# Performance work log

Hardware: AMD Instinct MI355X
Metric: run time of the kernel (lower is better)

Reference implementation:

```python
import jax, jax.numpy as jnp
import numpy as np

N_WORD, N_TOPIC, N_DOC = 50000, 2000, 50000
D_WORD, D_TOPIC, D_OUT = 256, 128, 128
E_WW, E_WT, E_WD, E_TD, E_TT = 500000, 400000, 500000, 400000, 300000


def setup_inputs() -> dict:
    key = jax.random.key(0)
    ks = jax.random.split(key, 32)
    i = iter(range(32))

    def randn(shape, scale=1.0):
        return jax.random.normal(ks[next(i)], shape, dtype=jnp.float32) * scale

    def edges(n_e, n_src, n_dst):
        src = jax.random.randint(ks[next(i)], (n_e,), 0, n_src, dtype=jnp.int32)
        dst = jax.random.randint(ks[next(i)], (n_e,), 0, n_dst, dtype=jnp.int32)
        w = jax.random.uniform(ks[next(i)], (n_e,), dtype=jnp.float32)
        return src, dst, w

    feat_word = randn((N_WORD, D_WORD))
    feat_topic = randn((N_TOPIC, D_TOPIC))
    ww_src, ww_dst, ww_w = edges(E_WW, N_WORD, N_WORD)
    wt_src, wt_dst, wt_w = edges(E_WT, N_WORD, N_TOPIC)
    wd_src, wd_dst, wd_w = edges(E_WD, N_WORD, N_DOC)
    td_src, td_dst, td_w = edges(E_TD, N_TOPIC, N_DOC)
    tt_src, tt_dst, tt_w = edges(E_TT, N_TOPIC, N_TOPIC)
    return dict(
        feat_word=feat_word, feat_topic=feat_topic,
        ww_src=ww_src, ww_dst=ww_dst, ww_w=ww_w,
        wt_src=wt_src, wt_dst=wt_dst, wt_w=wt_w,
        wd_src=wd_src, wd_dst=wd_dst, wd_w=wd_w,
        td_src=td_src, td_dst=td_dst, td_w=td_w,
        tt_src=tt_src, tt_dst=tt_dst, tt_w=tt_w,
        W_ww=randn((D_WORD, D_OUT), 0.02), b_ww=randn((D_OUT,), 0.02),
        W_wt=randn((D_WORD, D_OUT), 0.02), b_wt=randn((D_OUT,), 0.02),
        W_wd=randn((D_WORD, D_OUT), 0.02), b_wd=randn((D_OUT,), 0.02),
        W_td=randn((D_TOPIC, D_OUT), 0.02), b_td=randn((D_OUT,), 0.02),
        W_tt=randn((D_TOPIC, D_OUT), 0.02), b_tt=randn((D_OUT,), 0.02),
    )


def _mean_agg(Wh, src, dst, w, n_dst):
    # u_mul_e: gather src feature, scale by edge weight; fn.mean: divide by in-degree
    m = Wh[src] * w[:, None]                                   # [E, D_OUT]
    s = jax.ops.segment_sum(m, dst, num_segments=n_dst)        # [n_dst, D_OUT]
    deg = jax.ops.segment_sum(jnp.ones_like(w), dst, num_segments=n_dst)
    return jnp.where(deg[:, None] > 0, s / jnp.maximum(deg, 1.0)[:, None], 0.0)


def reference(feat_word, feat_topic,
              ww_src, ww_dst, ww_w, wt_src, wt_dst, wt_w,
              wd_src, wd_dst, wd_w, td_src, td_dst, td_w,
              tt_src, tt_dst, tt_w,
              W_ww, b_ww, W_wt, b_wt, W_wd, b_wd, W_td, b_td, W_tt, b_tt):
    # Per-relation projections (note: in the torch source the causal/noise
    # branches are overwritten by the plain Linear, so this is the effective math).
    Wh_ww = feat_word @ W_ww + b_ww
    Wh_wt = feat_word @ W_wt + b_wt
    Wh_wd = feat_word @ W_wd + b_wd
    Wh_td = feat_topic @ W_td + b_td
    Wh_tt = feat_topic @ W_tt + b_tt
    # mean per edge type, then cross-etype 'sum' per destination node type
    h_word = _mean_agg(Wh_ww, ww_src, ww_dst, ww_w, N_WORD)
    h_topic = (_mean_agg(Wh_wt, wt_src, wt_dst, wt_w, N_TOPIC)
               + _mean_agg(Wh_tt, tt_src, tt_dst, tt_w, N_TOPIC))
    h_doc = (_mean_agg(Wh_wd, wd_src, wd_dst, wd_w, N_DOC)
             + _mean_agg(Wh_td, td_src, td_dst, td_w, N_DOC))
    return h_word, h_topic, h_doc
```

## Files before the change

### kernel.cpp

```cpp
#include <hip/hip_runtime.h>

typedef short short8 __attribute__((ext_vector_type(8)));
typedef float floatx4 __attribute__((ext_vector_type(4)));

__device__ __forceinline__ float b2f(unsigned int u16) {
    union { unsigned int i; float f; } v;
    v.i = u16 << 16;
    return v.f;
}
__device__ __forceinline__ unsigned short f2b(float f) {
    unsigned int i = __float_as_uint(f);
    unsigned int r = (i + 0x7FFFu + ((i >> 16) & 1u)) >> 16;
    return (unsigned short)r;
}

#define N_WORD  50000
#define N_TOPIC 2000
#define N_DOC   50000
#define CHAIN_END 0xFFFFFFFFu
#define NB_GEMM 814
#define NSLOT_WW (N_WORD * 8)
#define NSLOT_WT (N_TOPIC * 4)
#define NSLOT_TT (N_TOPIC * 4)
#define NSLOT_WD (N_DOC * 8)
#define NSLOT_TD (N_DOC * 8)
#define NSLOT_ALL (NSLOT_WW + NSLOT_WT + NSLOT_TT + NSLOT_WD + NSLOT_TD)

__global__ void detect_kernel(const unsigned int* __restrict__ feat_u32,
                              unsigned int* __restrict__ flag)
{
    int cnt = 0;
    for (int i = 0; i < 256; ++i) {
        unsigned int u = feat_u32[i];
        int e = (u >> 7) & 0xFF;
        if (e >= 110 && e <= 140) ++cnt;
    }
    *flag = (cnt > 128) ? 1u : 0u;
}

__global__ __launch_bounds__(256) void swizzle_kernel(
    const void* __restrict__ W0, const void* __restrict__ W1,
    const void* __restrict__ W2, const void* __restrict__ W3,
    const void* __restrict__ W4,
    const void* __restrict__ b0, const void* __restrict__ b1,
    const void* __restrict__ b2, const void* __restrict__ b3,
    const void* __restrict__ b4,
    short8* __restrict__ D0, short8* __restrict__ D1,
    short8* __restrict__ D2, short8* __restrict__ D3,
    short8* __restrict__ D4,
    unsigned short* __restrict__ bias_out,
    const unsigned int* __restrict__ flag_p)
{
    const int w = blockIdx.y;
    const void* W; const void* bs; short8* D; int S;
    switch (w) {
        case 0: W = W0; bs = b0; D = D0; S = 8; break;
        case 1: W = W1; bs = b1; D = D1; S = 8; break;
        case 2: W = W2; bs = b2; D = D2; S = 8; break;
        case 3: W = W3; bs = b3; D = D3; S = 4; break;
        default: W = W4; bs = b4; D = D4; S = 4; break;
    }
    const int n_entries = S * 8 * 64;
    const int mode = (int)*flag_p;
    for (int e = blockIdx.x * 256 + threadIdx.x; e < n_entries; e += 8 * 256) {
        const int lane = e & 63, t = (e >> 6) & 7, s = e >> 9;
        const int q = lane >> 4, n = t * 16 + (lane & 15);
        short8 val;
#pragma unroll
        for (int j = 0; j < 8; ++j) {
            const int k = s * 32 + q * 8 + j;
            unsigned short hv = mode ? ((const unsigned short*)W)[k * 128 + n]
                                     : f2b(((const float*)W)[k * 128 + n]);
            val[j] = (short)hv;
        }
        D[e] = val;
    }
    if (blockIdx.x == 0 && threadIdx.x < 128) {
        bias_out[w * 128 + threadIdx.x] =
            mode ? ((const unsigned short*)bs)[threadIdx.x]
                 : f2b(((const float*)bs)[threadIdx.x]);
    }
}

template <int S, int NP>
__device__ __forceinline__ void gemm_body_lds(
    short8* __restrict__ Blds,
    const void* feat_, int n_rows, int bx,
    const short8* Ba, const short8* Bb, const short8* Bc,
    const unsigned short* bias_all, int ba, int bb, int bc,
    unsigned short* Oa, unsigned short* Ob, unsigned short* Oc,
    int mode_bf16)
{
    const int tid = threadIdx.x;
    const int lane = tid & 63;
    const int wave = tid >> 6;
    const int row0 = (bx * 4 + wave) * 16;
    const int m = lane & 15, q = lane >> 4;
    const int K = S * 32;
    int arow_idx = row0 + m;
    if (arow_idx >= n_rows) arow_idx = n_rows - 1;

    short8 a[S];
    if (mode_bf16) {
        const short8* arow = (const short8*)((const unsigned short*)feat_ + (size_t)arow_idx * K);
#pragma unroll
        for (int s = 0; s < S; ++s) a[s] = arow[s * 4 + q];
    } else {
        const float* arow = (const float*)feat_ + (size_t)arow_idx * K;
#pragma unroll
        for (int s = 0; s < S; ++s) {
            const float4 f0 = ((const float4*)arow)[s * 8 + q * 2];
            const float4 f1 = ((const float4*)arow)[s * 8 + q * 2 + 1];
            short8 t;
            t[0] = (short)f2b(f0.x); t[1] = (short)f2b(f0.y);
            t[2] = (short)f2b(f0.z); t[3] = (short)f2b(f0.w);
            t[4] = (short)f2b(f1.x); t[5] = (short)f2b(f1.y);
            t[6] = (short)f2b(f1.z); t[7] = (short)f2b(f1.w);
            a[s] = t;
        }
    }

    constexpr int NH = (S * 8 * 64 > 2048) ? 2 : 1;
    constexpr int SH = S / NH;

#pragma unroll
    for (int p = 0; p < NP; ++p) {
        const short8* B = (p == 0) ? Ba : ((p == 1) ? Bb : Bc);
        const unsigned short* bias = bias_all + ((p == 0) ? ba : ((p == 1) ? bb : bc)) * 128;
        unsigned short* O = (p == 0) ? Oa : ((p == 1) ? Ob : Oc);

        floatx4 acc[8];
#pragma unroll
        for (int t = 0; t < 8; ++t) { acc[t][0] = 0.f; acc[t][1] = 0.f; acc[t][2] = 0.f; acc[t][3] = 0.f; }

#pragma unroll
        for (int h = 0; h < NH; ++h) {
            __syncthreads();
            for (int i = tid; i < SH * 8 * 64; i += 256) Blds[i] = B[h * (SH * 8 * 64) + i];
            __syncthreads();
#pragma unroll
            for (int s = 0; s < SH; ++s) {
#pragma unroll
                for (int t = 0; t < 8; ++t) {
                    short8 b = Blds[(s * 8 + t) * 64 + lane];
                    acc[t] = __builtin_amdgcn_mfma_f32_16x16x32_bf16(a[h * SH + s], b, acc[t], 0, 0, 0);
                }
            }
        }

#pragma unroll
        for (int t = 0; t < 8; ++t) {
            const float bb_ = b2f((unsigned int)bias[t * 16 + m]);
#pragma unroll
            for (int r = 0; r < 4; ++r) {
                const int row = row0 + q * 4 + r;
                if (row < n_rows)
                    O[(size_t)row * 128 + t * 16 + m] = f2b(acc[t][r] + bb_);
            }
        }
    }
}

__global__ __launch_bounds__(256) void link_gemm_kernel(
    const void* __restrict__ feat_word, const void* __restrict__ feat_topic,
    const short8* __restrict__ Bww, const short8* __restrict__ Bwt,
    const short8* __restrict__ Bwd, const short8* __restrict__ Btt,
    const short8* __restrict__ Btd,
    const unsigned short* __restrict__ bias_all,
    unsigned short* __restrict__ Wh_ww, unsigned short* __restrict__ Wh_wt,
    unsigned short* __restrict__ Wh_wd, unsigned short* __restrict__ Wh_tt,
    unsigned short* __restrict__ Wh_td,
    const int* s0, const int* d0, const void* w0, int n0, unsigned int* h0, unsigned long long* e0,
    const int* s1, const int* d1, const void* w1, int n1, unsigned int* h1, unsigned long long* e1,
    const int* s2, const int* d2, const void* w2, int n2, unsigned int* h2, unsigned long long* e2,
    const int* s3, const int* d3, const void* w3, int n3, unsigned int* h3, unsigned long long* e3,
    const int* s4, const int* d4, const void* w4, int n4, unsigned int* h4, unsigned long long* e4,
    const unsigned int* __restrict__ flag_p)
{
    __shared__ short8 Blds[2048];
    const int mode = (int)*flag_p;

    if (blockIdx.x < NB_GEMM) {
        if (blockIdx.x < 782) {
            gemm_body_lds<8, 3>(Blds, feat_word, N_WORD, blockIdx.x, Bww, Bwt, Bwd,
                                bias_all, 0, 1, 2, Wh_ww, Wh_wt, Wh_wd, mode);
        } else {
            gemm_body_lds<4, 2>(Blds, feat_topic, N_TOPIC, blockIdx.x - 782, Btt, Btd,
                                (const short8*)nullptr, bias_all, 4, 3, 0,
                                Wh_tt, Wh_td, (unsigned short*)nullptr, mode);
        }
        return;
    }

    int lb = blockIdx.x - NB_GEMM;
    const int nb0 = (n0 + 255) >> 8, nb1 = (n1 + 255) >> 8, nb2 = (n2 + 255) >> 8,
              nb3 = (n3 + 255) >> 8;
    const int* src; const int* dst; const void* w_; int n;
    unsigned int* head; unsigned long long* ent; int H;
    if (lb < nb0)      { src = s0; dst = d0; w_ = w0; n = n0; head = h0; ent = e0; H = 8; }
    else if ((lb -= nb0) < nb1) { src = s1; dst = d1; w_ = w1; n = n1; head = h1; ent = e1; H = 4; }
    else if ((lb -= nb1) < nb2) { src = s2; dst = d2; w_ = w2; n = n2; head = h2; ent = e2; H = 4; }
    else if ((lb -= nb2) < nb3) { src = s3; dst = d3; w_ = w3; n = n3; head = h3; ent = e3; H = 8; }
    else { lb -= nb3;  src = s4; dst = d4; w_ = w4; n = n4; head = h4; ent = e4; H = 8; }

    const int i = lb * 256 + threadIdx.x;
    if (i >= n) return;
    const int d = dst[i];
    const unsigned int slot = (unsigned int)d * H + ((unsigned int)i & (H - 1));
    const unsigned int old = atomicExch(&head[slot], (unsigned int)i);
    const unsigned short w16 = mode ? ((const unsigned short*)w_)[i]
                                    : f2b(((const float*)w_)[i]);
    ent[i] = ((unsigned long long)old << 32)
           | ((unsigned long long)w16 << 16)
           | (unsigned long long)(unsigned int)src[i];
}

__device__ __forceinline__ void acc8(float a[8], const uint4& u, float w)
{
    a[0] += b2f(u.x & 0xffffu) * w; a[1] += b2f(u.x >> 16) * w;
    a[2] += b2f(u.y & 0xffffu) * w; a[3] += b2f(u.y >> 16) * w;
    a[4] += b2f(u.z & 0xffffu) * w; a[5] += b2f(u.z >> 16) * w;
    a[6] += b2f(u.w & 0xffffu) * w; a[7] += b2f(u.w >> 16) * w;
}
__device__ __forceinline__ uint4 rowld(const unsigned short* Wh, unsigned long long v, int sl)
{
    return ((const uint4*)(Wh + (size_t)((unsigned int)v & 0xffffu) * 128))[sl];
}

__device__ __forceinline__ void walk2s(
    const unsigned long long* __restrict__ ent, const unsigned short* __restrict__ Wh,
    unsigned int e1, unsigned int e2, int sl, float a[8], float& cnt)
{
    bool l1 = (e1 != CHAIN_END), l2 = (e2 != CHAIN_END);
    unsigned long long v1 = 0, v2 = 0;
    if (l1) v1 = ent[e1];
    if (l2) v2 = ent[e2];
    while (l1 || l2) {
        const unsigned int n1 = (unsigned int)(v1 >> 32);
        const unsigned int n2 = (unsigned int)(v2 >> 32);
        const bool l1n = l1 && (n1 != CHAIN_END);
        const bool l2n = l2 && (n2 != CHAIN_END);
        unsigned long long v1n = 0, v2n = 0;
        if (l1n) v1n = ent[n1];
        if (l2n) v2n = ent[n2];
        uint4 u1, u2;
        if (l1) u1 = rowld(Wh, v1, sl);
        if (l2) u2 = rowld(Wh, v2, sl);
        if (l1) { acc8(a, u1, b2f(((unsigned int)v1) >> 16)); cnt += 1.0f; }
        if (l2) { acc8(a, u2, b2f(((unsigned int)v2) >> 16)); cnt += 1.0f; }
        v1 = v1n; v2 = v2n; l1 = l1n; l2 = l2n;
    }
}

__device__ __forceinline__ void walk2(
    const unsigned long long* __restrict__ ent1, const unsigned short* __restrict__ Wh1, unsigned int e1,
    const unsigned long long* __restrict__ ent2, const unsigned short* __restrict__ Wh2, unsigned int e2,
    int sl, float a1[8], float a2[8], float& c1, float& c2)
{
    bool l1 = (e1 != CHAIN_END), l2 = (e2 != CHAIN_END);
    unsigned long long v1 = 0, v2 = 0;
    if (l1) v1 = ent1[e1];
    if (l2) v2 = ent2[e2];
    while (l1 || l2) {
        const unsigned int n1 = (unsigned int)(v1 >> 32);
        const unsigned int n2 = (unsigned int)(v2 >> 32);
        const bool l1n = l1 && (n1 != CHAIN_END);
        const bool l2n = l2 && (n2 != CHAIN_END);
        unsigned long long v1n = 0, v2n = 0;
        if (l1n) v1n = ent1[n1];
        if (l2n) v2n = ent2[n2];
        uint4 u1, u2;
        if (l1) u1 = rowld(Wh1, v1, sl);
        if (l2) u2 = rowld(Wh2, v2, sl);
        if (l1) { acc8(a1, u1, b2f(((unsigned int)v1) >> 16)); c1 += 1.0f; }
        if (l2) { acc8(a2, u2, b2f(((unsigned int)v2) >> 16)); c2 += 1.0f; }
        v1 = v1n; v2 = v2n; l1 = l1n; l2 = l2n;
    }
}

__device__ __forceinline__ void walk4(
    const unsigned long long* __restrict__ entA, const unsigned short* __restrict__ WhA,
    unsigned int ea1, unsigned int ea2,
    const unsigned long long* __restrict__ entB, const unsigned short* __restrict__ WhB,
    unsigned int eb1, unsigned int eb2,
    int sl, float a1[8], float a2[8], float& c1, float& c2)
{
    bool la1 = (ea1 != CHAIN_END), la2 = (ea2 != CHAIN_END);
    bool lb1 = (eb1 != CHAIN_END), lb2 = (eb2 != CHAIN_END);
    unsigned long long va1 = 0, va2 = 0, vb1 = 0, vb2 = 0;
    if (la1) va1 = entA[ea1];
    if (la2) va2 = entA[ea2];
    if (lb1) vb1 = entB[eb1];
    if (lb2) vb2 = entB[eb2];
    while (la1 || la2 || lb1 || lb2) {
        const unsigned int na1 = (unsigned int)(va1 >> 32);
        const unsigned int na2 = (unsigned int)(va2 >> 32);
        const unsigned int nb1 = (unsigned int)(vb1 >> 32);
        const unsigned int nb2 = (unsigned int)(vb2 >> 32);
        const bool la1n = la1 && (na1 != CHAIN_END);
        const bool la2n = la2 && (na2 != CHAIN_END);
        const bool lb1n = lb1 && (nb1 != CHAIN_END);
        const bool lb2n = lb2 && (nb2 != CHAIN_END);
        unsigned long long va1n = 0, va2n = 0, vb1n = 0, vb2n = 0;
        if (la1n) va1n = entA[na1];
        if (la2n) va2n = entA[na2];
        if (lb1n) vb1n = entB[nb1];
        if (lb2n) vb2n = entB[nb2];
        uint4 ua1, ua2, ub1, ub2;
        if (la1) ua1 = rowld(WhA, va1, sl);
        if (la2) ua2 = rowld(WhA, va2, sl);
        if (lb1) ub1 = rowld(WhB, vb1, sl);
        if (lb2) ub2 = rowld(WhB, vb2, sl);
        if (la1) { acc8(a1, ua1, b2f(((unsigned int)va1) >> 16)); c1 += 1.0f; }
        if (la2) { acc8(a1, ua2, b2f(((unsigned int)va2) >> 16)); c1 += 1.0f; }
        if (lb1) { acc8(a2, ub1, b2f(((unsigned int)vb1) >> 16)); c2 += 1.0f; }
        if (lb2) { acc8(a2, ub2, b2f(((unsigned int)vb2) >> 16)); c2 += 1.0f; }
        va1 = va1n; va2 = va2n; vb1 = vb1n; vb2 = vb2n;
        la1 = la1n; la2 = la2n; lb1 = lb1n; lb2 = lb2n;
    }
}

__device__ __forceinline__ void write8(
    void* out, size_t off_elems, int node, int sl, const float r[8], int mode)
{
    if (mode) {
        uint4 o;
        o.x = (unsigned int)f2b(r[0]) | ((unsigned int)f2b(r[1]) << 16);
        o.y = (unsigned int)f2b(r[2]) | ((unsigned int)f2b(r[3]) << 16);
        o.z = (unsigned int)f2b(r[4]) | ((unsigned int)f2b(r[5]) << 16);
        o.w = (unsigned int)f2b(r[6]) | ((unsigned int)f2b(r[7]) << 16);
        *(uint4*)((unsigned short*)out + off_elems + (size_t)node * 128 + sl * 8) = o;
    } else {
        float* p = (float*)out + off_elems + (size_t)node * 128 + sl * 8;
        ((float4*)p)[0] = make_float4(r[0], r[1], r[2], r[3]);
        ((float4*)p)[1] = make_float4(r[4], r[5], r[6], r[7]);
    }
}

__device__ __forceinline__ void topic_body(
    const unsigned int* __restrict__ h1, const unsigned long long* __restrict__ e1t,
    const unsigned short* __restrict__ Wh1,
    const unsigned int* __restrict__ h2, const unsigned long long* __restrict__ e2t,
    const unsigned short* __restrict__ Wh2,
    void* __restrict__ out, size_t off_elems, int blk, int mode)
{
    const int sl = threadIdx.x & 15;
    const int grp = (threadIdx.x >> 4) & 3;
    const int wave = threadIdx.x >> 6;
    const int node = blk * 4 + wave;
    float a1[8] = {0,0,0,0,0,0,0,0}, a2[8] = {0,0,0,0,0,0,0,0};
    float c1 = 0.f, c2 = 0.f;
    walk2(e1t, Wh1, h1[node * 4 + grp], e2t, Wh2, h2[node * 4 + grp],
          sl, a1, a2, c1, c2);
#pragma unroll
    for (int j = 0; j < 8; ++j) {
        a1[j] += __shfl_xor(a1[j], 16); a1[j] += __shfl_xor(a1[j], 32);
        a2[j] += __shfl_xor(a2[j], 16); a2[j] += __shfl_xor(a2[j], 32);
    }
    c1 += __shfl_xor(c1, 16); c1 += __shfl_xor(c1, 32);
    c2 += __shfl_xor(c2, 16); c2 += __shfl_xor(c2, 32);
    const float i1 = (c1 > 0.f) ? 1.f / c1 : 0.f;
    const float i2 = (c2 > 0.f) ? 1.f / c2 : 0.f;
    float r[8];
#pragma unroll
    for (int j = 0; j < 8; ++j) r[j] = a1[j] * i1 + a2[j] * i2;
    if (grp == 0) write8(out, off_elems, node, sl, r, mode);
}

__device__ __forceinline__ void doc_body(
    const unsigned int* __restrict__ h1, const unsigned long long* __restrict__ e1t,
    const unsigned short* __restrict__ Wh1,
    const unsigned int* __restrict__ h2, const unsigned long long* __restrict__ e2t,
    const unsigned short* __restrict__ Wh2,
    void* __restrict__ out, size_t off_elems, int blk, int mode)
{
    const int sl = threadIdx.x & 15;
    const int grp = (threadIdx.x >> 4) & 3;
    const int wave = threadIdx.x >> 6;
    const int node = blk * 4 + wave;
    float a1[8] = {0,0,0,0,0,0,0,0}, a2[8] = {0,0,0,0,0,0,0,0};
    float c1 = 0.f, c2 = 0.f;
    walk4(e1t, Wh1, h1[node * 8 + grp * 2], h1[node * 8 + grp * 2 + 1],
          e2t, Wh2, h2[node * 8 + grp * 2], h2[node * 8 + grp * 2 + 1],
          sl, a1, a2, c1, c2);
#pragma unroll
    for (int j = 0; j < 8; ++j) {
        a1[j] += __shfl_xor(a1[j], 16); a1[j] += __shfl_xor(a1[j], 32);
        a2[j] += __shfl_xor(a2[j], 16); a2[j] += __shfl_xor(a2[j], 32);
    }
    c1 += __shfl_xor(c1, 16); c1 += __shfl_xor(c1, 32);
    c2 += __shfl_xor(c2, 16); c2 += __shfl_xor(c2, 32);
    const float i1 = (c1 > 0.f) ? 1.f / c1 : 0.f;
    const float i2 = (c2 > 0.f) ? 1.f / c2 : 0.f;
    float r[8];
#pragma unroll
    for (int j = 0; j < 8; ++j) r[j] = a1[j] * i1 + a2[j] * i2;
    if (grp == 0) write8(out, off_elems, node, sl, r, mode);
}

__device__ __forceinline__ void word_body(
    const unsigned int* __restrict__ h_ww, const unsigned long long* __restrict__ e_ww,
    const unsigned short* __restrict__ Wh_ww,
    void* __restrict__ out, int blk, int mode)
{
    const int sl = threadIdx.x & 15;
    const int grp = (threadIdx.x >> 4) & 3;
    const int wave = threadIdx.x >> 6;
    const int node = blk * 4 + wave;
    float a[8] = {0,0,0,0,0,0,0,0}; float cnt = 0.f;
    walk2s(e_ww, Wh_ww, h_ww[node * 8 + grp * 2], h_ww[node * 8 + grp * 2 + 1],
           sl, a, cnt);
#pragma unroll
    for (int j = 0; j < 8; ++j) { a[j] += __shfl_xor(a[j], 16); a[j] += __shfl_xor(a[j], 32); }
    cnt += __shfl_xor(cnt, 16); cnt += __shfl_xor(cnt, 32);
    const float inv = (cnt > 0.f) ? 1.f / cnt : 0.f;
    float r[8];
#pragma unroll
    for (int j = 0; j < 8; ++j) r[j] = a[j] * inv;
    if (grp == 0) write8(out, 0, node, sl, r, mode);
}

__global__ __launch_bounds__(256) void gather_all_kernel(
    const unsigned int* __restrict__ h_wt, const unsigned long long* __restrict__ e_wt,
    const unsigned short* __restrict__ Wh_wt,
    const unsigned int* __restrict__ h_tt, const unsigned long long* __restrict__ e_tt,
    const unsigned short* __restrict__ Wh_tt,
    const unsigned int* __restrict__ h_wd, const unsigned long long* __restrict__ e_wd,
    const unsigned short* __restrict__ Wh_wd,
    const unsigned int* __restrict__ h_td, const unsigned long long* __restrict__ e_td,
    const unsigned short* __restrict__ Wh_td,
    const unsigned int* __restrict__ h_ww, const unsigned long long* __restrict__ e_ww,
    const unsigned short* __restrict__ Wh_ww,
    void* __restrict__ out,
    const unsigned int* __restrict__ flag_p)
{
    const int mode = (int)*flag_p;
    if (blockIdx.x < 500) {
        topic_body(h_wt, e_wt, Wh_wt, h_tt, e_tt, Wh_tt,
                   out, (size_t)6400000, blockIdx.x, mode);
    } else if (blockIdx.x < 13000) {
        doc_body(h_wd, e_wd, Wh_wd, h_td, e_td, Wh_td,
                 out, (size_t)6656000, blockIdx.x - 500, mode);
    } else {
        word_body(h_ww, e_ww, Wh_ww, out, blockIdx.x - 13000, mode);
    }
}

__global__ __launch_bounds__(256) void gather_dt_kernel(
    const unsigned int* __restrict__ h_wt, const unsigned long long* __restrict__ e_wt,
    const unsigned short* __restrict__ Wh_wt,
    const unsigned int* __restrict__ h_tt, const unsigned long long* __restrict__ e_tt,
    const unsigned short* __restrict__ Wh_tt,
    const unsigned int* __restrict__ h_wd, const unsigned long long* __restrict__ e_wd,
    const unsigned short* __restrict__ Wh_wd,
    const unsigned int* __restrict__ h_td, const unsigned long long* __restrict__ e_td,
    const unsigned short* __restrict__ Wh_td,
    void* __restrict__ out,
    const unsigned int* __restrict__ flag_p)
{
    const int mode = (int)*flag_p;
    if (blockIdx.x < 500) {
        topic_body(h_wt, e_wt, Wh_wt, h_tt, e_tt, Wh_tt,
                   out, (size_t)6400000, blockIdx.x, mode);
    } else {
        doc_body(h_wd, e_wd, Wh_wd, h_td, e_td, Wh_td,
                 out, (size_t)6656000, blockIdx.x - 500, mode);
    }
}

__global__ __launch_bounds__(256) void gather_w_kernel(
    const unsigned int* __restrict__ h_ww, const unsigned long long* __restrict__ e_ww,
    const unsigned short* __restrict__ Wh_ww,
    void* __restrict__ out,
    const unsigned int* __restrict__ flag_p)
{
    word_body(h_ww, e_ww, Wh_ww, out, blockIdx.x, (int)*flag_p);
}

extern "C" void kernel_launch(void* const* d_in, const int* in_sizes, int n_in,
                              void* d_out, int out_size, void* d_ws, size_t ws_size,
                              hipStream_t stream)
{
    const void* feat_word  = d_in[0];
    const void* feat_topic = d_in[1];
    const int* ww_src = (const int*)d_in[2];
    const int* ww_dst = (const int*)d_in[3];
    const void* ww_w = d_in[4];
    const int* wt_src = (const int*)d_in[5];
    const int* wt_dst = (const int*)d_in[6];
    const void* wt_w = d_in[7];
    const int* wd_src = (const int*)d_in[8];
    const int* wd_dst = (const int*)d_in[9];
    const void* wd_w = d_in[10];
    const int* td_src = (const int*)d_in[11];
    const int* td_dst = (const int*)d_in[12];
    const void* td_w = d_in[13];
    const int* tt_src = (const int*)d_in[14];
    const int* tt_dst = (const int*)d_in[15];
    const void* tt_w = d_in[16];
    const void* W_ww = d_in[17];
    const void* b_ww = d_in[18];
    const void* W_wt = d_in[19];
    const void* b_wt = d_in[20];
    const void* W_wd = d_in[21];
    const void* b_wd = d_in[22];
    const void* W_td = d_in[23];
    const void* b_td = d_in[24];
    const void* W_tt = d_in[25];
    const void* b_tt = d_in[26];

    const int E_ww = in_sizes[2];
    const int E_wt = in_sizes[5];
    const int E_wd = in_sizes[8];
    const int E_td = in_sizes[11];
    const int E_tt = in_sizes[14];

    char* ws = (char*)d_ws;
    unsigned int* flag = (unsigned int*)ws;
    unsigned int* head_base = (unsigned int*)(ws + 4);
    unsigned int* h_ww = head_base;
    unsigned int* h_wt = h_ww + NSLOT_WW;
    unsigned int* h_tt = h_wt + NSLOT_WT;
    unsigned int* h_wd = h_tt + NSLOT_TT;
    unsigned int* h_td = h_wd + NSLOT_WD;
    size_t off = 4 + (size_t)NSLOT_ALL * 4;
    off = (off + 15) & ~(size_t)15;
    short8* Bsw_ww = (short8*)(ws + off); off += 65536;
    short8* Bsw_wt = (short8*)(ws + off); off += 65536;
    short8* Bsw_wd = (short8*)(ws + off); off += 65536;
    short8* Bsw_td = (short8*)(ws + off); off += 32768;
    short8* Bsw_tt = (short8*)(ws + off); off += 32768;
    unsigned short* bias_all = (unsigned short*)(ws + off); off += 5 * 128 * 2;
    off = (off + 15) & ~(size_t)15;
    unsigned short* Wh_ww = (unsigned short*)(ws + off); off += (size_t)N_WORD * 128 * 2;
    unsigned short* Wh_wt = (unsigned short*)(ws + off); off += (size_t)N_WORD * 128 * 2;
    unsigned short* Wh_tt = (unsigned short*)(ws + off); off += (size_t)N_TOPIC * 128 * 2;
    unsigned short* Wh_td = (unsigned short*)(ws + off); off += (size_t)N_TOPIC * 128 * 2;
    off = (off + 7) & ~(size_t)7;
    unsigned long long* e_ww = (unsigned long long*)(ws + off); off += (size_t)E_ww * 8;
    unsigned long long* e_wt = (unsigned long long*)(ws + off); off += (size_t)E_wt * 8;
    unsigned long long* e_tt = (unsigned long long*)(ws + off); off += (size_t)E_tt * 8;
    unsigned long long* e_wd = (unsigned long long*)(ws + off); off += (size_t)E_wd * 8;
    unsigned long long* e_td = (unsigned long long*)(ws + off); off += (size_t)E_td * 8;

    off = (off + 15) & ~(size_t)15;
    const size_t whwd_bytes = (size_t)N_WORD * 128 * 2;
    const bool fuse_gather = (ws_size >= off + whwd_bytes);
    unsigned short* Wh_wd = fuse_gather ? (unsigned short*)(ws + off)
                                        : (unsigned short*)d_out;

    detect_kernel<<<1, 1, 0, stream>>>((const unsigned int*)feat_word, flag);
    hipMemsetAsync(head_base, 0xFF, (size_t)NSLOT_ALL * 4, stream);

    swizzle_kernel<<<dim3(8, 5), 256, 0, stream>>>(
        W_ww, W_wt, W_wd, W_td, W_tt, b_ww, b_wt, b_wd, b_td, b_tt,
        Bsw_ww, Bsw_wt, Bsw_wd, Bsw_td, Bsw_tt, bias_all, flag);

    const int nb_link = ((E_ww + 255) / 256) + ((E_wt + 255) / 256) +
                        ((E_tt + 255) / 256) + ((E_wd + 255) / 256) +
                        ((E_td + 255) / 256);
    link_gemm_kernel<<<NB_GEMM + nb_link, 256, 0, stream>>>(
        feat_word, feat_topic, Bsw_ww, Bsw_wt, Bsw_wd, Bsw_tt, Bsw_td,
        bias_all, Wh_ww, Wh_wt, Wh_wd, Wh_tt, Wh_td,
        ww_src, ww_dst, ww_w, E_ww, h_ww, e_ww,
        wt_src, wt_dst, wt_w, E_wt, h_wt, e_wt,
        tt_src, tt_dst, tt_w, E_tt, h_tt, e_tt,
        wd_src, wd_dst, wd_w, E_wd, h_wd, e_wd,
        td_src, td_dst, td_w, E_td, h_td, e_td, flag);

    if (fuse_gather) {
        gather_all_kernel<<<500 + 12500 + 12500, 256, 0, stream>>>(
            h_wt, e_wt, Wh_wt, h_tt, e_tt, Wh_tt,
            h_wd, e_wd, Wh_wd, h_td, e_td, Wh_td,
            h_ww, e_ww, Wh_ww, d_out, flag);
    } else {
        gather_dt_kernel<<<500 + 12500, 256, 0, stream>>>(
            h_wt, e_wt, Wh_wt, h_tt, e_tt, Wh_tt,
            h_wd, e_wd, Wh_wd, h_td, e_td, Wh_td, d_out, flag);
        gather_w_kernel<<<12500, 256, 0, stream>>>(
            h_ww, e_ww, Wh_ww, d_out, flag);
    }
}
```

Measured before the change: 384.2 us.

## Stage Wh_wt in output buffer, split topic gather, halve doc chain heads

```diff
diff --git a/kernel.cpp b/kernel.cpp
--- a/kernel.cpp
+++ b/kernel.cpp
@@ -22,8 +22,8 @@
 #define NSLOT_WW (N_WORD * 8)
 #define NSLOT_WT (N_TOPIC * 4)
 #define NSLOT_TT (N_TOPIC * 4)
-#define NSLOT_WD (N_DOC * 8)
-#define NSLOT_TD (N_DOC * 8)
+#define NSLOT_WD (N_DOC * 4)
+#define NSLOT_TD (N_DOC * 4)
 #define NSLOT_ALL (NSLOT_WW + NSLOT_WT + NSLOT_TT + NSLOT_WD + NSLOT_TD)
 
 __global__ void detect_kernel(const unsigned int* __restrict__ feat_u32,
@@ -200,8 +200,8 @@
     if (lb < nb0)      { src = s0; dst = d0; w_ = w0; n = n0; head = h0; ent = e0; H = 8; }
     else if ((lb -= nb0) < nb1) { src = s1; dst = d1; w_ = w1; n = n1; head = h1; ent = e1; H = 4; }
     else if ((lb -= nb1) < nb2) { src = s2; dst = d2; w_ = w2; n = n2; head = h2; ent = e2; H = 4; }
-    else if ((lb -= nb2) < nb3) { src = s3; dst = d3; w_ = w3; n = n3; head = h3; ent = e3; H = 8; }
-    else { lb -= nb3;  src = s4; dst = d4; w_ = w4; n = n4; head = h4; ent = e4; H = 8; }
+    else if ((lb -= nb2) < nb3) { src = s3; dst = d3; w_ = w3; n = n3; head = h3; ent = e3; H = 4; }
+    else { lb -= nb3;  src = s4; dst = d4; w_ = w4; n = n4; head = h4; ent = e4; H = 4; }
 
     const int i = lb * 256 + threadIdx.x;
     if (i >= n) return;
@@ -222,9 +222,9 @@
     a[4] += b2f(u.z & 0xffffu) * w; a[5] += b2f(u.z >> 16) * w;
     a[6] += b2f(u.w & 0xffffu) * w; a[7] += b2f(u.w >> 16) * w;
 }
-__device__ __forceinline__ uint4 rowld(const unsigned short* Wh, unsigned long long v, int sl)
-{
-    return ((const uint4*)(Wh + (size_t)((unsigned int)v & 0xffffu) * 128))[sl];
+__device__ __forceinline__ uint4 rowld(const unsigned short* Wh, unsigned int pay, int sl)
+{
+    return ((const uint4*)(Wh + (size_t)(pay & 0xffffu) * 128))[sl];
 }
 
 __device__ __forceinline__ void walk2s(
@@ -244,8 +244,8 @@
         if (l1n) v1n = ent[n1];
         if (l2n) v2n = ent[n2];
         uint4 u1, u2;
-        if (l1) u1 = rowld(Wh, v1, sl);
-        if (l2) u2 = rowld(Wh, v2, sl);
+        if (l1) u1 = rowld(Wh, (unsigned int)v1, sl);
+        if (l2) u2 = rowld(Wh, (unsigned int)v2, sl);
         if (l1) { acc8(a, u1, b2f(((unsigned int)v1) >> 16)); cnt += 1.0f; }
         if (l2) { acc8(a, u2, b2f(((unsigned int)v2) >> 16)); cnt += 1.0f; }
         v1 = v1n; v2 = v2n; l1 = l1n; l2 = l2n;
@@ -270,53 +270,11 @@
         if (l1n) v1n = ent1[n1];
         if (l2n) v2n = ent2[n2];
         uint4 u1, u2;
-        if (l1) u1 = rowld(Wh1, v1, sl);
-        if (l2) u2 = rowld(Wh2, v2, sl);
+        if (l1) u1 = rowld(Wh1, (unsigned int)v1, sl);
+        if (l2) u2 = rowld(Wh2, (unsigned int)v2, sl);
         if (l1) { acc8(a1, u1, b2f(((unsigned int)v1) >> 16)); c1 += 1.0f; }
         if (l2) { acc8(a2, u2, b2f(((unsigned int)v2) >> 16)); c2 += 1.0f; }
         v1 = v1n; v2 = v2n; l1 = l1n; l2 = l2n;
-    }
-}
-
-__device__ __forceinline__ void walk4(
-    const unsigned long long* __restrict__ entA, const unsigned short* __restrict__ WhA,
-    unsigned int ea1, unsigned int ea2,
-    const unsigned long long* __restrict__ entB, const unsigned short* __restrict__ WhB,
-    unsigned int eb1, unsigned int eb2,
-    int sl, float a1[8], float a2[8], float& c1, float& c2)
-{
-    bool la1 = (ea1 != CHAIN_END), la2 = (ea2 != CHAIN_END);
-    bool lb1 = (eb1 != CHAIN_END), lb2 = (eb2 != CHAIN_END);
-    unsigned long long va1 = 0, va2 = 0, vb1 = 0, vb2 = 0;
-    if (la1) va1 = entA[ea1];
-    if (la2) va2 = entA[ea2];
-    if (lb1) vb1 = entB[eb1];
-    if (lb2) vb2 = entB[eb2];
-    while (la1 || la2 || lb1 || lb2) {
-        const unsigned int na1 = (unsigned int)(va1 >> 32);
-        const unsigned int na2 = (unsigned int)(va2 >> 32);
-        const unsigned int nb1 = (unsigned int)(vb1 >> 32);
-        const unsigned int nb2 = (unsigned int)(vb2 >> 32);
-        const bool la1n = la1 && (na1 != CHAIN_END);
-        const bool la2n = la2 && (na2 != CHAIN_END);
-        const bool lb1n = lb1 && (nb1 != CHAIN_END);
-        const bool lb2n = lb2 && (nb2 != CHAIN_END);
-        unsigned long long va1n = 0, va2n = 0, vb1n = 0, vb2n = 0;
-        if (la1n) va1n = entA[na1];
-        if (la2n) va2n = entA[na2];
-        if (lb1n) vb1n = entB[nb1];
-        if (lb2n) vb2n = entB[nb2];
-        uint4 ua1, ua2, ub1, ub2;
-        if (la1) ua1 = rowld(WhA, va1, sl);
-        if (la2) ua2 = rowld(WhA, va2, sl);
-        if (lb1) ub1 = rowld(WhB, vb1, sl);
-        if (lb2) ub2 = rowld(WhB, vb2, sl);
-        if (la1) { acc8(a1, ua1, b2f(((unsigned int)va1) >> 16)); c1 += 1.0f; }
-        if (la2) { acc8(a1, ua2, b2f(((unsigned int)va2) >> 16)); c1 += 1.0f; }
-        if (lb1) { acc8(a2, ub1, b2f(((unsigned int)vb1) >> 16)); c2 += 1.0f; }
-        if (lb2) { acc8(a2, ub2, b2f(((unsigned int)vb2) >> 16)); c2 += 1.0f; }
-        va1 = va1n; va2 = va2n; vb1 = vb1n; vb2 = vb2n;
-        la1 = la1n; la2 = la2n; lb1 = lb1n; lb2 = lb2n;
     }
 }
 
@@ -337,20 +295,22 @@
     }
 }
 
-__device__ __forceinline__ void topic_body(
-    const unsigned int* __restrict__ h1, const unsigned long long* __restrict__ e1t,
-    const unsigned short* __restrict__ Wh1,
-    const unsigned int* __restrict__ h2, const unsigned long long* __restrict__ e2t,
-    const unsigned short* __restrict__ Wh2,
-    void* __restrict__ out, size_t off_elems, int blk, int mode)
-{
+__global__ __launch_bounds__(256) void gather_topic_kernel(
+    const unsigned int* __restrict__ h_wt, const unsigned long long* __restrict__ e_wt,
+    const unsigned short* __restrict__ Wh_wt,
+    const unsigned int* __restrict__ h_tt, const unsigned long long* __restrict__ e_tt,
+    const unsigned short* __restrict__ Wh_tt,
+    void* __restrict__ out,
+    const unsigned int* __restrict__ flag_p)
+{
+    const int mode = (int)*flag_p;
     const int sl = threadIdx.x & 15;
     const int grp = (threadIdx.x >> 4) & 3;
     const int wave = threadIdx.x >> 6;
-    const int node = blk * 4 + wave;
+    const int node = blockIdx.x * 4 + wave;
     float a1[8] = {0,0,0,0,0,0,0,0}, a2[8] = {0,0,0,0,0,0,0,0};
     float c1 = 0.f, c2 = 0.f;
-    walk2(e1t, Wh1, h1[node * 4 + grp], e2t, Wh2, h2[node * 4 + grp],
+    walk2(e_wt, Wh_wt, h_wt[node * 4 + grp], e_tt, Wh_tt, h_tt[node * 4 + grp],
           sl, a1, a2, c1, c2);
 #pragma unroll
     for (int j = 0; j < 8; ++j) {
@@ -364,67 +324,10 @@
     float r[8];
 #pragma unroll
     for (int j = 0; j < 8; ++j) r[j] = a1[j] * i1 + a2[j] * i2;
-    if (grp == 0) write8(out, off_elems, node, sl, r, mode);
-}
-
-__device__ __forceinline__ void doc_body(
-    const unsigned int* __restrict__ h1, const unsigned long long* __restrict__ e1t,
-    const unsigned short* __restrict__ Wh1,
-    const unsigned int* __restrict__ h2, const unsigned long long* __restrict__ e2t,
-    const unsigned short* __restrict__ Wh2,
-    void* __restrict__ out, size_t off_elems, int blk, int mode)
-{
-    const int sl = threadIdx.x & 15;
-    const int grp = (threadIdx.x >> 4) & 3;
-    const int wave = threadIdx.x >> 6;
-    const int node = blk * 4 + wave;
-    float a1[8] = {0,0,0,0,0,0,0,0}, a2[8] = {0,0,0,0,0,0,0,0};
-    float c1 = 0.f, c2 = 0.f;
-    walk4(e1t, Wh1, h1[node * 8 + grp * 2], h1[node * 8 + grp * 2 + 1],
-          e2t, Wh2, h2[node * 8 + grp * 2], h2[node * 8 + grp * 2 + 1],
-          sl, a1, a2, c1, c2);
-#pragma unroll
-    for (int j = 0; j < 8; ++j) {
-        a1[j] += __shfl_xor(a1[j], 16); a1[j] += __shfl_xor(a1[j], 32);
-        a2[j] += __shfl_xor(a2[j], 16); a2[j] += __shfl_xor(a2[j], 32);
-    }
-    c1 += __shfl_xor(c1, 16); c1 += __shfl_xor(c1, 32);
-    c2 += __shfl_xor(c2, 16); c2 += __shfl_xor(c2, 32);
-    const float i1 = (c1 > 0.f) ? 1.f / c1 : 0.f;
-    const float i2 = (c2 > 0.f) ? 1.f / c2 : 0.f;
-    float r[8];
-#pragma unroll
-    for (int j = 0; j < 8; ++j) r[j] = a1[j] * i1 + a2[j] * i2;
-    if (grp == 0) write8(out, off_elems, node, sl, r, mode);
-}
-
-__device__ __forceinline__ void word_body(
-    const unsigned int* __restrict__ h_ww, const unsigned long long* __restrict__ e_ww,
-    const unsigned short* __restrict__ Wh_ww,
-    void* __restrict__ out, int blk, int mode)
-{
-    const int sl = threadIdx.x & 15;
-    const int grp = (threadIdx.x >> 4) & 3;
-    const int wave = threadIdx.x >> 6;
-    const int node = blk * 4 + wave;
-    float a[8] = {0,0,0,0,0,0,0,0}; float cnt = 0.f;
-    walk2s(e_ww, Wh_ww, h_ww[node * 8 + grp * 2], h_ww[node * 8 + grp * 2 + 1],
-           sl, a, cnt);
-#pragma unroll
-    for (int j = 0; j < 8; ++j) { a[j] += __shfl_xor(a[j], 16); a[j] += __shfl_xor(a[j], 32); }
-    cnt += __shfl_xor(cnt, 16); cnt += __shfl_xor(cnt, 32);
-    const float inv = (cnt > 0.f) ? 1.f / cnt : 0.f;
-    float r[8];
-#pragma unroll
-    for (int j = 0; j < 8; ++j) r[j] = a[j] * inv;
-    if (grp == 0) write8(out, 0, node, sl, r, mode);
-}
-
-__global__ __launch_bounds__(256) void gather_all_kernel(
-    const unsigned int* __restrict__ h_wt, const unsigned long long* __restrict__ e_wt,
-    const unsigned short* __restrict__ Wh_wt,
-    const unsigned int* __restrict__ h_tt, const unsigned long long* __restrict__ e_tt,
-    const unsigned short* __restrict__ Wh_tt,
+    if (grp == 0) write8(out, (size_t)6400000, node, sl, r, mode);
+}
+
+__global__ __launch_bounds__(256) void gather_dw_kernel(
     const unsigned int* __restrict__ h_wd, const unsigned long long* __restrict__ e_wd,
     const unsigned short* __restrict__ Wh_wd,
     const unsigned int* __restrict__ h_td, const unsigned long long* __restrict__ e_td,
@@ -435,46 +338,43 @@
     const unsigned int* __restrict__ flag_p)
 {
     const int mode = (int)*flag_p;
-    if (blockIdx.x < 500) {
-        topic_body(h_wt, e_wt, Wh_wt, h_tt, e_tt, Wh_tt,
-                   out, (size_t)6400000, blockIdx.x, mode);
-    } else if (blockIdx.x < 13000) {
-        doc_body(h_wd, e_wd, Wh_wd, h_td, e_td, Wh_td,
-                 out, (size_t)6656000, blockIdx.x - 500, mode);
+    const int sl = threadIdx.x & 15;
+    const int grp = (threadIdx.x >> 4) & 3;
+    const int wave = threadIdx.x >> 6;
+
+    if (blockIdx.x < 12500) {
+        const int node = blockIdx.x * 4 + wave;
+        float a1[8] = {0,0,0,0,0,0,0,0}, a2[8] = {0,0,0,0,0,0,0,0};
+        float c1 = 0.f, c2 = 0.f;
+        walk2(e_wd, Wh_wd, h_wd[node * 4 + grp], e_td, Wh_td, h_td[node * 4 + grp],
+              sl, a1, a2, c1, c2);
+#pragma unroll
+        for (int j = 0; j < 8; ++j) {
+            a1[j] += __shfl_xor(a1[j], 16); a1[j] += __shfl_xor(a1[j], 32);
+            a2[j] += __shfl_xor(a2[j], 16); a2[j] += __shfl_xor(a2[j], 32);
+        }
+        c1 += __shfl_xor(c1, 16); c1 += __shfl_xor(c1, 32);
+        c2 += __shfl_xor(c2, 16); c2 += __shfl_xor(c2, 32);
+        const float i1 = (c1 > 0.f) ? 1.f / c1 : 0.f;
+        const float i2 = (c2 > 0.f) ? 1.f / c2 : 0.f;
+        float r[8];
+#pragma unroll
+        for (int j = 0; j < 8; ++j) r[j] = a1[j] * i1 + a2[j] * i2;
+        if (grp == 0) write8(out, (size_t)6656000, node, sl, r, mode);
     } else {
-        word_body(h_ww, e_ww, Wh_ww, out, blockIdx.x - 13000, mode);
-    }
-}
-
-__global__ __launch_bounds__(256) void gather_dt_kernel(
-    const unsigned int* __restrict__ h_wt, const unsigned long long* __restrict__ e_wt,
-    const unsigned short* __restrict__ Wh_wt,
-    const unsigned int* __restrict__ h_tt, const unsigned long long* __restrict__ e_tt,
-    const unsigned short* __restrict__ Wh_tt,
-    const unsigned int* __restrict__ h_wd, const unsigned long long* __restrict__ e_wd,
-    const unsigned short* __restrict__ Wh_wd,
-    const unsigned int* __restrict__ h_td, const unsigned long long* __restrict__ e_td,
-    const unsigned short* __restrict__ Wh_td,
-    void* __restrict__ out,
-    const unsigned int* __restrict__ flag_p)
-{
-    const int mode = (int)*flag_p;
-    if (blockIdx.x < 500) {
-        topic_body(h_wt, e_wt, Wh_wt, h_tt, e_tt, Wh_tt,
-                   out, (size_t)6400000, blockIdx.x, mode);
-    } else {
-        doc_body(h_wd, e_wd, Wh_wd, h_td, e_td, Wh_td,
-                 out, (size_t)6656000, blockIdx.x - 500, mode);
-    }
-}
-
-__global__ __launch_bounds__(256) void gather_w_kernel(
-    const unsigned int* __restrict__ h_ww, const unsigned long long* __restrict__ e_ww,
-    const unsigned short* __restrict__ Wh_ww,
-    void* __restrict__ out,
-    const unsigned int* __restrict__ flag_p)
-{
-    word_body(h_ww, e_ww, Wh_ww, out, blockIdx.x, (int)*flag_p);
+        const int node = (blockIdx.x - 12500) * 4 + wave;
+        float a[8] = {0,0,0,0,0,0,0,0}; float cnt = 0.f;
+        walk2s(e_ww, Wh_ww, h_ww[node * 8 + grp * 2], h_ww[node * 8 + grp * 2 + 1],
+               sl, a, cnt);
+#pragma unroll
+        for (int j = 0; j < 8; ++j) { a[j] += __shfl_xor(a[j], 16); a[j] += __shfl_xor(a[j], 32); }
+        cnt += __shfl_xor(cnt, 16); cnt += __shfl_xor(cnt, 32);
+        const float inv = (cnt > 0.f) ? 1.f / cnt : 0.f;
+        float r[8];
+#pragma unroll
+        for (int j = 0; j < 8; ++j) r[j] = a[j] * inv;
+        if (grp == 0) write8(out, 0, node, sl, r, mode);
+    }
 }
 
 extern "C" void kernel_launch(void* const* d_in, const int* in_sizes, int n_in,
@@ -517,13 +417,13 @@
 
     char* ws = (char*)d_ws;
     unsigned int* flag = (unsigned int*)ws;
-    unsigned int* head_base = (unsigned int*)(ws + 4);
+    unsigned int* head_base = (unsigned int*)(ws + 16);
     unsigned int* h_ww = head_base;
     unsigned int* h_wt = h_ww + NSLOT_WW;
     unsigned int* h_tt = h_wt + NSLOT_WT;
     unsigned int* h_wd = h_tt + NSLOT_TT;
     unsigned int* h_td = h_wd + NSLOT_WD;
-    size_t off = 4 + (size_t)NSLOT_ALL * 4;
+    size_t off = 16 + (size_t)NSLOT_ALL * 4;
     off = (off + 15) & ~(size_t)15;
     short8* Bsw_ww = (short8*)(ws + off); off += 65536;
     short8* Bsw_wt = (short8*)(ws + off); off += 65536;
@@ -533,7 +433,7 @@
     unsigned short* bias_all = (unsigned short*)(ws + off); off += 5 * 128 * 2;
     off = (off + 15) & ~(size_t)15;
     unsigned short* Wh_ww = (unsigned short*)(ws + off); off += (size_t)N_WORD * 128 * 2;
-    unsigned short* Wh_wt = (unsigned short*)(ws + off); off += (size_t)N_WORD * 128 * 2;
+    unsigned short* Wh_wd = (unsigned short*)(ws + off); off += (size_t)N_WORD * 128 * 2;
     unsigned short* Wh_tt = (unsigned short*)(ws + off); off += (size_t)N_TOPIC * 128 * 2;
     unsigned short* Wh_td = (unsigned short*)(ws + off); off += (size_t)N_TOPIC * 128 * 2;
     off = (off + 7) & ~(size_t)7;
@@ -543,11 +443,7 @@
     unsigned long long* e_wd = (unsigned long long*)(ws + off); off += (size_t)E_wd * 8;
     unsigned long long* e_td = (unsigned long long*)(ws + off); off += (size_t)E_td * 8;
 
-    off = (off + 15) & ~(size_t)15;
-    const size_t whwd_bytes = (size_t)N_WORD * 128 * 2;
-    const bool fuse_gather = (ws_size >= off + whwd_bytes);
-    unsigned short* Wh_wd = fuse_gather ? (unsigned short*)(ws + off)
-                                        : (unsigned short*)d_out;
+    unsigned short* Wh_wt = (unsigned short*)d_out;
 
     detect_kernel<<<1, 1, 0, stream>>>((const unsigned int*)feat_word, flag);
     hipMemsetAsync(head_base, 0xFF, (size_t)NSLOT_ALL * 4, stream);
@@ -568,16 +464,10 @@
         wd_src, wd_dst, wd_w, E_wd, h_wd, e_wd,
         td_src, td_dst, td_w, E_td, h_td, e_td, flag);
 
-    if (fuse_gather) {
-        gather_all_kernel<<<500 + 12500 + 12500, 256, 0, stream>>>(
-            h_wt, e_wt, Wh_wt, h_tt, e_tt, Wh_tt,
-            h_wd, e_wd, Wh_wd, h_td, e_td, Wh_td,
-            h_ww, e_ww, Wh_ww, d_out, flag);
-    } else {
-        gather_dt_kernel<<<500 + 12500, 256, 0, stream>>>(
-            h_wt, e_wt, Wh_wt, h_tt, e_tt, Wh_tt,
-            h_wd, e_wd, Wh_wd, h_td, e_td, Wh_td, d_out, flag);
-        gather_w_kernel<<<12500, 256, 0, stream>>>(
-            h_ww, e_ww, Wh_ww, d_out, flag);
-    }
-}
+    gather_topic_kernel<<<500, 256, 0, stream>>>(
+        h_wt, e_wt, Wh_wt, h_tt, e_tt, Wh_tt, d_out, flag);
+
+    gather_dw_kernel<<<25000, 256, 0, stream>>>(
+        h_wd, e_wd, Wh_wd, h_td, e_td, Wh_td,
+        h_ww, e_ww, Wh_ww, d_out, flag);
+}
```

Result: slower. 402.9 us (+4.9%).
